# Kernel optimization log

Hardware: AMD Instinct MI355X
Metric: run time of the kernel (lower is better)

Reference implementation:

```python
import jax, jax.numpy as jnp
import numpy as np

IN_F = 128
OUT_F = 64
ALPHA = 0.2  # LeakyReLU negative slope


def setup_inputs() -> dict:
    key = jax.random.key(0)
    k1, k2, k3 = jax.random.split(key, 3)
    B, N = 8, 2048
    inp = jax.random.normal(k1, (B, N, IN_F), dtype=jnp.float32)
    adj = jnp.ones((B, N, N), dtype=jnp.float32)  # unused by the layer (no masking)
    # Parameters (xavier_uniform-style scale)
    w_lim = np.sqrt(6.0 / (IN_F + OUT_F))
    W = jax.random.uniform(k2, (OUT_F, IN_F), minval=-w_lim, maxval=w_lim, dtype=jnp.float32)
    a_lim = np.sqrt(6.0 / (2 * OUT_F + 1))
    a = jax.random.uniform(k3, (1, 2 * OUT_F), minval=-a_lim, maxval=a_lim, dtype=jnp.float32)
    return {"input": inp, "adj": adj, "W": W, "a": a}


def reference(input, adj, W, a):
    # h = W(input): [B, N, OUT_F]
    h = jnp.einsum("bnf,of->bno", input, W)
    # a^T [h_i || h_j] = a1^T h_i + a2^T h_j  (exact decomposition of the concat trick)
    a1 = a[0, :OUT_F]
    a2 = a[0, OUT_F:]
    s1 = jnp.einsum("bno,o->bn", h, a1)  # score contribution from node i
    s2 = jnp.einsum("bno,o->bn", h, a2)  # score contribution from node j
    e = s1[:, :, None] + s2[:, None, :]  # [B, N, N]
    e = jnp.where(e >= 0, e, ALPHA * e)  # LeakyReLU
    attention = jax.nn.softmax(e, axis=2)  # softmax over neighbors j (adj is NOT used)
    h_prime = jnp.einsum("bij,bjo->bio", attention, h)
    # concat=True -> ELU
    return jax.nn.elu(h_prime)
```

## Files before the change

kernel.cpp:

```cpp
#include <hip/hip_runtime.h>
#include <cstdio>

#define ALPHA 0.2f
constexpr int NN = 2048;
constexpr int NB = 8;
constexpr int FI = 128;
constexpr int FO = 64;
constexpr int SEG = 16;
constexpr int NSEG = NN / SEG;

__global__ __launch_bounds__(256) void k_h(const float* __restrict__ inp,
    const float* __restrict__ W, const float* __restrict__ a,
    float* __restrict__ h, float* __restrict__ s1, float* __restrict__ s2)
{
  __shared__ float4 Wq[(FI / 4) * FO];
  const int t = threadIdx.x;
  const float4* Wg = (const float4*)W;
#pragma unroll
  for (int i = 0; i < 8; ++i) {
    int f = t + i * 256;
    Wq[(f & 31) * FO + (f >> 5)] = Wg[f];
  }
  __syncthreads();
  const int lane = t & 63;
  const int wv = t >> 6;
  const size_t rowbase = ((size_t)blockIdx.x * 4 + wv) * 8;
  const float a1v = a[lane], a2v = a[FO + lane];
#pragma unroll
  for (int g = 0; g < 2; ++g) {
    const size_t r0 = rowbase + g * 4;
    const float4* x0 = (const float4*)(inp + r0 * FI);
    const float4* x1 = x0 + (FI / 4);
    const float4* x2 = x0 + 2 * (FI / 4);
    const float4* x3 = x0 + 3 * (FI / 4);
    float acc0 = 0.f, acc1 = 0.f, acc2 = 0.f, acc3 = 0.f;
#pragma unroll
    for (int cq = 0; cq < 32; ++cq) {
      float4 w = Wq[cq * FO + lane];
      float4 xa = x0[cq];
      acc0 = fmaf(xa.x, w.x, fmaf(xa.y, w.y, fmaf(xa.z, w.z, fmaf(xa.w, w.w, acc0))));
      float4 xb = x1[cq];
      acc1 = fmaf(xb.x, w.x, fmaf(xb.y, w.y, fmaf(xb.z, w.z, fmaf(xb.w, w.w, acc1))));
      float4 xc = x2[cq];
      acc2 = fmaf(xc.x, w.x, fmaf(xc.y, w.y, fmaf(xc.z, w.z, fmaf(xc.w, w.w, acc2))));
      float4 xd = x3[cq];
      acc3 = fmaf(xd.x, w.x, fmaf(xd.y, w.y, fmaf(xd.z, w.z, fmaf(xd.w, w.w, acc3))));
    }
    h[(r0 + 0) * FO + lane] = acc0;
    h[(r0 + 1) * FO + lane] = acc1;
    h[(r0 + 2) * FO + lane] = acc2;
    h[(r0 + 3) * FO + lane] = acc3;
    float p0 = acc0 * a1v, q0 = acc0 * a2v;
    float p1 = acc1 * a1v, q1 = acc1 * a2v;
    float p2 = acc2 * a1v, q2 = acc2 * a2v;
    float p3 = acc3 * a1v, q3 = acc3 * a2v;
#pragma unroll
    for (int off = 32; off; off >>= 1) {
      p0 += __shfl_down(p0, off); q0 += __shfl_down(q0, off);
      p1 += __shfl_down(p1, off); q1 += __shfl_down(q1, off);
      p2 += __shfl_down(p2, off); q2 += __shfl_down(q2, off);
      p3 += __shfl_down(p3, off); q3 += __shfl_down(q3, off);
    }
    if (lane == 0) {
      s1[r0 + 0] = p0; s2[r0 + 0] = q0;
      s1[r0 + 1] = p1; s2[r0 + 1] = q1;
      s1[r0 + 2] = p2; s2[r0 + 2] = q2;
      s1[r0 + 3] = p3; s2[r0 + 3] = q3;
    }
  }
}

__global__ __launch_bounds__(512) void k_count(
    const float* __restrict__ s1g, const float* __restrict__ s2g,
    int* __restrict__ sortedIdx, float* __restrict__ epS,
    float* __restrict__ eqS, int* __restrict__ kArr,
    float* __restrict__ zpArr, float* __restrict__ zqArr,
    float* __restrict__ m2g)
{
  __shared__ float sv[NN];
  __shared__ float sepA[NN], seqA[NN];
  __shared__ float wmx[8];
  __shared__ int   prk[64 * 8], pkk[64 * 8];
  __shared__ float pzp[64 * 8], pzq[64 * 8];
  const int b = blockIdx.x >> 5;
  const int c = blockIdx.x & 31;
  const int t = threadIdx.x;
  const int lane = t & 63;
  const int wv = t >> 6;
  float4* sv4 = (float4*)sv;
  const float4* g4 = (const float4*)(s2g + (size_t)b * NN);
  const float4 mine = g4[t];
  sv4[t] = mine;
  float mx = fmaxf(fmaxf(mine.x, mine.y), fmaxf(mine.z, mine.w));
#pragma unroll
  for (int off = 32; off; off >>= 1) mx = fmaxf(mx, __shfl_down(mx, off));
  if (lane == 0) wmx[wv] = mx;
  __syncthreads();
  float m2 = wmx[0];
#pragma unroll
  for (int i = 1; i < 8; ++i) m2 = fmaxf(m2, wmx[i]);
  if (c == 0 && t == 0) m2g[b] = m2;
  {
    float4 e1, e2;
    e1.x = expf(mine.x - m2); e2.x = expf(ALPHA * (mine.x - m2));
    e1.y = expf(mine.y - m2); e2.y = expf(ALPHA * (mine.y - m2));
    e1.z = expf(mine.z - m2); e2.z = expf(ALPHA * (mine.z - m2));
    e1.w = expf(mine.w - m2); e2.w = expf(ALPHA * (mine.w - m2));
    ((float4*)sepA)[t] = e1;
    ((float4*)seqA)[t] = e2;
  }
  __syncthreads();
  const int ib = c * 64 + lane;
  const float v = sv[ib];
  const float thr = -s1g[(size_t)b * NN + ib];
  int cR0 = 0, cR1 = 0, cK0 = 0, cK1 = 0;
  float zp0 = 0.f, zp1 = 0.f, zq0 = 0.f, zq1 = 0.f;
  const float4* svv = (const float4*)sv;
  const float4* epv = (const float4*)sepA;
  const float4* eqv = (const float4*)seqA;
#pragma unroll 4
  for (int j4 = wv * 64; j4 < wv * 64 + 64; ++j4) {
    const float4 x = svv[j4];
    const float4 e1 = epv[j4];
    const float4 e2 = eqv[j4];
    const int j = 4 * j4;
    bool p0 = (x.x >= thr), p1 = (x.y >= thr), p2 = (x.z >= thr), p3 = (x.w >= thr);
    cK0 += p0 + p1; cK1 += p2 + p3;
    zp0 += (p0 ? e1.x : 0.f) + (p1 ? e1.y : 0.f);
    zp1 += (p2 ? e1.z : 0.f) + (p3 ? e1.w : 0.f);
    zq0 += (p0 ? 0.f : e2.x) + (p1 ? 0.f : e2.y);
    zq1 += (p2 ? 0.f : e2.z) + (p3 ? 0.f : e2.w);
    cR0 += ((x.x > v) || (x.x == v && (j + 0) < ib))
         + ((x.y > v) || (x.y == v && (j + 1) < ib));
    cR1 += ((x.z > v) || (x.z == v && (j + 2) < ib))
         + ((x.w > v) || (x.w == v && (j + 3) < ib));
  }
  prk[lane * 8 + wv] = cR0 + cR1;
  pkk[lane * 8 + wv] = cK0 + cK1;
  pzp[lane * 8 + wv] = zp0 + zp1;
  pzq[lane * 8 + wv] = zq0 + zq1;
  __syncthreads();
  if (t < 64) {
    int rank = 0, kk = 0;
    float zps = 0.f, zqs = 0.f;
#pragma unroll
    for (int i2 = 0; i2 < 8; ++i2) {
      rank += prk[t * 8 + i2]; kk += pkk[t * 8 + i2];
      zps += pzp[t * 8 + i2]; zqs += pzq[t * 8 + i2];
    }
    const int i = c * 64 + t;
    kArr[b * NN + i] = kk;
    zpArr[b * NN + i] = zps;
    zqArr[b * NN + i] = zqs;
    sortedIdx[b * NN + rank] = i;
    epS[b * NN + rank] = sepA[i];
    eqS[b * NN + rank] = seqA[i];
  }
}

__global__ __launch_bounds__(256) void k_seg(const float* __restrict__ h,
    const int* __restrict__ sortedIdx, const float* __restrict__ epS,
    const float* __restrict__ eqS,
    float* __restrict__ Lp, float* __restrict__ Lq,
    float* __restrict__ segTotP, float* __restrict__ segTotQ)
{
  const int lane = threadIdx.x & 63;
  const int s = blockIdx.x * 4 + (threadIdx.x >> 6);
  const int b = s >> 7;
  const int base = b * NN + (s & (NSEG - 1)) * SEG;
  float hv[SEG], wp[SEG], wq[SEG];
#pragma unroll
  for (int r = 0; r < SEG; ++r) {
    int idx = sortedIdx[base + r];
    hv[r] = h[((size_t)(b * NN + idx)) * FO + lane];
  }
#pragma unroll
  for (int r = 0; r < SEG; ++r) { wp[r] = epS[base + r]; wq[r] = eqS[base + r]; }
  float run = 0.f;
#pragma unroll
  for (int r = 0; r < SEG; ++r) {
    run = fmaf(wp[r], hv[r], run);
    Lp[(size_t)(base + r) * FO + lane] = run;
  }
  segTotP[(size_t)s * FO + lane] = run;
  run = 0.f;
#pragma unroll
  for (int r = SEG - 1; r >= 0; --r) {
    run = fmaf(wq[r], hv[r], run);
    Lq[(size_t)(base + r) * FO + lane] = run;
  }
  segTotQ[(size_t)s * FO + lane] = run;
}

__global__ __launch_bounds__(256) void k_out(const float* __restrict__ s1g,
    const int* __restrict__ kArr, const float* __restrict__ zpArr,
    const float* __restrict__ zqArr,
    const float* __restrict__ Lp, const float* __restrict__ Lq,
    const float* __restrict__ segTotP, const float* __restrict__ segTotQ,
    const float* __restrict__ m2g, float* __restrict__ out)
{
  __shared__ float cs[NSEG * FO];
  __shared__ float qt[4][FO];
  const int t = threadIdx.x;
  const int b = blockIdx.x >> 5;
  const int c = blockIdx.x & 31;
  const int lane = t & 63;
  const int wv = t >> 6;
  int kk[16];
#pragma unroll
  for (int rr = 0; rr < 16; ++rr)
    kk[rr] = kArr[b * NN + c * 64 + wv * 16 + rr];

  {
    const float4* sv4 = (const float4*)(segTotP + (size_t)b * NSEG * FO);
    float4* csv = (float4*)cs;
#pragma unroll
    for (int i = 0; i < NSEG * FO / 4 / 256; ++i) csv[t + i * 256] = sv4[t + i * 256];
  }
  __syncthreads();
  {
    float run = 0.f;
    for (int s = wv * 32; s < wv * 32 + 32; ++s) { run += cs[s * FO + lane]; cs[s * FO + lane] = run; }
    qt[wv][lane] = run;
  }
  __syncthreads();
  {
    float off = 0.f;
    for (int q2 = 0; q2 < wv; ++q2) off += qt[q2][lane];
    for (int s = wv * 32; s < wv * 32 + 32; ++s) cs[s * FO + lane] += off;
  }
  __syncthreads();
  float P[16];
#pragma unroll
  for (int rr = 0; rr < 16; ++rr) {
    const int k = kk[rr];
    P[rr] = 0.f;
    if (k > 0) {
      const int sP = (k - 1) >> 4;
      P[rr] = (sP > 0 ? cs[(sP - 1) * FO + lane] : 0.f) +
              Lp[((size_t)(b * NN + k - 1)) * FO + lane];
    }
  }
  __syncthreads();

  {
    const float4* sv4 = (const float4*)(segTotQ + (size_t)b * NSEG * FO);
    float4* csv = (float4*)cs;
#pragma unroll
    for (int i = 0; i < NSEG * FO / 4 / 256; ++i) csv[t + i * 256] = sv4[t + i * 256];
  }
  __syncthreads();
  {
    float run = 0.f;
    for (int s = wv * 32 + 31; s >= wv * 32; --s) { run += cs[s * FO + lane]; cs[s * FO + lane] = run; }
    qt[wv][lane] = run;
  }
  __syncthreads();
  {
    float off = 0.f;
    for (int q2 = wv + 1; q2 < 4; ++q2) off += qt[q2][lane];
    for (int s = wv * 32; s < wv * 32 + 32; ++s) cs[s * FO + lane] += off;
  }
  __syncthreads();
  float Q[16];
#pragma unroll
  for (int rr = 0; rr < 16; ++rr) {
    const int k = kk[rr];
    Q[rr] = 0.f;
    if (k < NN) {
      const int sQ = k >> 4;
      Q[rr] = (sQ < NSEG - 1 ? cs[(sQ + 1) * FO + lane] : 0.f) +
              Lq[((size_t)(b * NN + k)) * FO + lane];
    }
  }

  const float m2 = m2g[b];
#pragma unroll
  for (int rr = 0; rr < 16; ++rr) {
    const int i = c * 64 + wv * 16 + rr;
    const int gi = b * NN + i;
    const float u = s1g[gi] + m2;
    const float cmx = fmaxf(u, ALPHA * u);
    const float wp = expf(u - cmx);
    const float wq = expf(ALPHA * u - cmx);
    const float v = (wp * P[rr] + wq * Q[rr]) / (wp * zpArr[gi] + wq * zqArr[gi]);
    out[(size_t)gi * FO + lane] = (v > 0.f) ? v : expm1f(v);
  }
}

extern "C" void kernel_launch(void* const* d_in, const int* in_sizes, int n_in,
                              void* d_out, int out_size, void* d_ws, size_t ws_size,
                              hipStream_t stream) {
  const float* inp = (const float*)d_in[0];
  const float* W = (const float*)d_in[2];
  const float* a = (const float*)d_in[3];
  float* out = (float*)d_out;

  constexpr size_t NH = (size_t)NB * NN * FO;
  constexpr size_t NR = (size_t)NB * NN;
  constexpr size_t NST = (size_t)NB * NSEG * FO;
  constexpr size_t needFloats = 3 * NH + 8 * NR + 2 * NST + 8;
  if (ws_size < needFloats * sizeof(float)) {
    fprintf(stderr, "kernel_launch: ws too small (%zu < %zu)\n",
            ws_size, needFloats * sizeof(float));
    return;
  }
  float* ws = (float*)d_ws;
  float* h        = ws;
  float* Lp       = h + NH;
  float* Lq       = Lp + NH;
  float* s1       = Lq + NH;
  float* s2       = s1 + NR;
  int*   sortedIdx= (int*)(s2 + NR);
  float* epS      = (float*)(sortedIdx + NR);
  float* eqS      = epS + NR;
  int*   kArr     = (int*)(eqS + NR);
  float* zpArr    = (float*)(kArr + NR);
  float* zqArr    = zpArr + NR;
  float* segTotP  = zqArr + NR;
  float* segTotQ  = segTotP + NST;
  float* m2       = segTotQ + NST;

  k_h<<<512, 256, 0, stream>>>(inp, W, a, h, s1, s2);
  k_count<<<256, 512, 0, stream>>>(s1, s2, sortedIdx, epS, eqS,
                                   kArr, zpArr, zqArr, m2);
  k_seg<<<256, 256, 0, stream>>>(h, sortedIdx, epS, eqS, Lp, Lq,
                                 segTotP, segTotQ);
  k_out<<<256, 256, 0, stream>>>(s1, kArr, zpArr, zqArr, Lp, Lq,
                                 segTotP, segTotQ, m2, out);
}
```

Measured before the change: 69.57 us.

## Fold W into attention vectors and compute h inside segment scan kernel

The first kernel now precomputes W^T a1 and W^T a2 so the scores s1/s2 come from a 128-wide dot product per row, without building h. The full projection h is recomputed inside k_seg by gathering input rows in sorted order, which removes the h write and re-read. The per-row softmax normalisers zp/zq, previously accumulated in the O(N^2) count loop, are now taken from prefix and suffix sums of the sorted exp weights. This shrinks the count kernel's inner loop and removes its exp work. The cost is heavier gathered loads of 128-float input rows in k_seg and extra prefix-offset logic in k_out.

```diff
diff --git a/kernel.cpp b/kernel.cpp
--- a/kernel.cpp
+++ b/kernel.cpp
@@ -9,79 +9,50 @@
 constexpr int SEG = 16;
 constexpr int NSEG = NN / SEG;
 
-__global__ __launch_bounds__(256) void k_h(const float* __restrict__ inp,
+__global__ __launch_bounds__(256) void k_s12(const float* __restrict__ inp,
     const float* __restrict__ W, const float* __restrict__ a,
-    float* __restrict__ h, float* __restrict__ s1, float* __restrict__ s2)
+    float* __restrict__ s1, float* __restrict__ s2)
 {
-  __shared__ float4 Wq[(FI / 4) * FO];
+  __shared__ float sw1[FI], sw2[FI];
   const int t = threadIdx.x;
-  const float4* Wg = (const float4*)W;
-#pragma unroll
-  for (int i = 0; i < 8; ++i) {
-    int f = t + i * 256;
-    Wq[(f & 31) * FO + (f >> 5)] = Wg[f];
+  if (t < FI) {
+    float w1 = 0.f, w2 = 0.f;
+    for (int o = 0; o < FO; ++o) {
+      const float wof = W[o * FI + t];
+      w1 = fmaf(a[o], wof, w1);
+      w2 = fmaf(a[FO + o], wof, w2);
+    }
+    sw1[t] = w1; sw2[t] = w2;
   }
   __syncthreads();
   const int lane = t & 63;
   const int wv = t >> 6;
-  const size_t rowbase = ((size_t)blockIdx.x * 4 + wv) * 8;
-  const float a1v = a[lane], a2v = a[FO + lane];
-#pragma unroll
-  for (int g = 0; g < 2; ++g) {
-    const size_t r0 = rowbase + g * 4;
-    const float4* x0 = (const float4*)(inp + r0 * FI);
-    const float4* x1 = x0 + (FI / 4);
-    const float4* x2 = x0 + 2 * (FI / 4);
-    const float4* x3 = x0 + 3 * (FI / 4);
-    float acc0 = 0.f, acc1 = 0.f, acc2 = 0.f, acc3 = 0.f;
-#pragma unroll
-    for (int cq = 0; cq < 32; ++cq) {
-      float4 w = Wq[cq * FO + lane];
-      float4 xa = x0[cq];
-      acc0 = fmaf(xa.x, w.x, fmaf(xa.y, w.y, fmaf(xa.z, w.z, fmaf(xa.w, w.w, acc0))));
-      float4 xb = x1[cq];
-      acc1 = fmaf(xb.x, w.x, fmaf(xb.y, w.y, fmaf(xb.z, w.z, fmaf(xb.w, w.w, acc1))));
-      float4 xc = x2[cq];
-      acc2 = fmaf(xc.x, w.x, fmaf(xc.y, w.y, fmaf(xc.z, w.z, fmaf(xc.w, w.w, acc2))));
-      float4 xd = x3[cq];
-      acc3 = fmaf(xd.x, w.x, fmaf(xd.y, w.y, fmaf(xd.z, w.z, fmaf(xd.w, w.w, acc3))));
-    }
-    h[(r0 + 0) * FO + lane] = acc0;
-    h[(r0 + 1) * FO + lane] = acc1;
-    h[(r0 + 2) * FO + lane] = acc2;
-    h[(r0 + 3) * FO + lane] = acc3;
-    float p0 = acc0 * a1v, q0 = acc0 * a2v;
-    float p1 = acc1 * a1v, q1 = acc1 * a2v;
-    float p2 = acc2 * a1v, q2 = acc2 * a2v;
-    float p3 = acc3 * a1v, q3 = acc3 * a2v;
+  const float w1a = sw1[lane], w1b = sw1[lane + 64];
+  const float w2a = sw2[lane], w2b = sw2[lane + 64];
+  const size_t row0 = (size_t)blockIdx.x * 32 + wv * 8;
+#pragma unroll
+  for (int r = 0; r < 8; ++r) {
+    const float xa = inp[(row0 + r) * FI + lane];
+    const float xb = inp[(row0 + r) * FI + 64 + lane];
+    float p = fmaf(xa, w1a, xb * w1b);
+    float q = fmaf(xa, w2a, xb * w2b);
 #pragma unroll
     for (int off = 32; off; off >>= 1) {
-      p0 += __shfl_down(p0, off); q0 += __shfl_down(q0, off);
-      p1 += __shfl_down(p1, off); q1 += __shfl_down(q1, off);
-      p2 += __shfl_down(p2, off); q2 += __shfl_down(q2, off);
-      p3 += __shfl_down(p3, off); q3 += __shfl_down(q3, off);
-    }
-    if (lane == 0) {
-      s1[r0 + 0] = p0; s2[r0 + 0] = q0;
-      s1[r0 + 1] = p1; s2[r0 + 1] = q1;
-      s1[r0 + 2] = p2; s2[r0 + 2] = q2;
-      s1[r0 + 3] = p3; s2[r0 + 3] = q3;
-    }
+      p += __shfl_down(p, off);
+      q += __shfl_down(q, off);
+    }
+    if (lane == 0) { s1[row0 + r] = p; s2[row0 + r] = q; }
   }
 }
 
 __global__ __launch_bounds__(512) void k_count(
     const float* __restrict__ s1g, const float* __restrict__ s2g,
     int* __restrict__ sortedIdx, float* __restrict__ epS,
-    float* __restrict__ eqS, int* __restrict__ kArr,
-    float* __restrict__ zpArr, float* __restrict__ zqArr,
-    float* __restrict__ m2g)
+    float* __restrict__ eqS, int* __restrict__ kArr, float* __restrict__ m2g)
 {
   __shared__ float sv[NN];
-  __shared__ float sepA[NN], seqA[NN];
   __shared__ float wmx[8];
-  __shared__ int   prk[64 * 8], pkk[64 * 8];
-  __shared__ float pzp[64 * 8], pzq[64 * 8];
+  __shared__ int prk[64 * 8], pkk[64 * 8];
   const int b = blockIdx.x >> 5;
   const int c = blockIdx.x & 31;
   const int t = threadIdx.x;
@@ -100,107 +71,115 @@
 #pragma unroll
   for (int i = 1; i < 8; ++i) m2 = fmaxf(m2, wmx[i]);
   if (c == 0 && t == 0) m2g[b] = m2;
-  {
-    float4 e1, e2;
-    e1.x = expf(mine.x - m2); e2.x = expf(ALPHA * (mine.x - m2));
-    e1.y = expf(mine.y - m2); e2.y = expf(ALPHA * (mine.y - m2));
-    e1.z = expf(mine.z - m2); e2.z = expf(ALPHA * (mine.z - m2));
-    e1.w = expf(mine.w - m2); e2.w = expf(ALPHA * (mine.w - m2));
-    ((float4*)sepA)[t] = e1;
-    ((float4*)seqA)[t] = e2;
-  }
-  __syncthreads();
   const int ib = c * 64 + lane;
   const float v = sv[ib];
   const float thr = -s1g[(size_t)b * NN + ib];
-  int cR0 = 0, cR1 = 0, cK0 = 0, cK1 = 0;
-  float zp0 = 0.f, zp1 = 0.f, zq0 = 0.f, zq1 = 0.f;
+  int cR = 0, cK = 0;
   const float4* svv = (const float4*)sv;
-  const float4* epv = (const float4*)sepA;
-  const float4* eqv = (const float4*)seqA;
 #pragma unroll 4
   for (int j4 = wv * 64; j4 < wv * 64 + 64; ++j4) {
     const float4 x = svv[j4];
-    const float4 e1 = epv[j4];
-    const float4 e2 = eqv[j4];
     const int j = 4 * j4;
-    bool p0 = (x.x >= thr), p1 = (x.y >= thr), p2 = (x.z >= thr), p3 = (x.w >= thr);
-    cK0 += p0 + p1; cK1 += p2 + p3;
-    zp0 += (p0 ? e1.x : 0.f) + (p1 ? e1.y : 0.f);
-    zp1 += (p2 ? e1.z : 0.f) + (p3 ? e1.w : 0.f);
-    zq0 += (p0 ? 0.f : e2.x) + (p1 ? 0.f : e2.y);
-    zq1 += (p2 ? 0.f : e2.z) + (p3 ? 0.f : e2.w);
-    cR0 += ((x.x > v) || (x.x == v && (j + 0) < ib))
-         + ((x.y > v) || (x.y == v && (j + 1) < ib));
-    cR1 += ((x.z > v) || (x.z == v && (j + 2) < ib))
-         + ((x.w > v) || (x.w == v && (j + 3) < ib));
-  }
-  prk[lane * 8 + wv] = cR0 + cR1;
-  pkk[lane * 8 + wv] = cK0 + cK1;
-  pzp[lane * 8 + wv] = zp0 + zp1;
-  pzq[lane * 8 + wv] = zq0 + zq1;
+    cK += (x.x >= thr) + (x.y >= thr) + (x.z >= thr) + (x.w >= thr);
+    cR += ((x.x > v) || (x.x == v && (j + 0) < ib))
+        + ((x.y > v) || (x.y == v && (j + 1) < ib))
+        + ((x.z > v) || (x.z == v && (j + 2) < ib))
+        + ((x.w > v) || (x.w == v && (j + 3) < ib));
+  }
+  prk[lane * 8 + wv] = cR;
+  pkk[lane * 8 + wv] = cK;
   __syncthreads();
   if (t < 64) {
     int rank = 0, kk = 0;
-    float zps = 0.f, zqs = 0.f;
-#pragma unroll
-    for (int i2 = 0; i2 < 8; ++i2) {
-      rank += prk[t * 8 + i2]; kk += pkk[t * 8 + i2];
-      zps += pzp[t * 8 + i2]; zqs += pzq[t * 8 + i2];
-    }
+#pragma unroll
+    for (int i2 = 0; i2 < 8; ++i2) { rank += prk[t * 8 + i2]; kk += pkk[t * 8 + i2]; }
     const int i = c * 64 + t;
+    const float vv = sv[i];
     kArr[b * NN + i] = kk;
-    zpArr[b * NN + i] = zps;
-    zqArr[b * NN + i] = zqs;
     sortedIdx[b * NN + rank] = i;
-    epS[b * NN + rank] = sepA[i];
-    eqS[b * NN + rank] = seqA[i];
-  }
-}
-
-__global__ __launch_bounds__(256) void k_seg(const float* __restrict__ h,
-    const int* __restrict__ sortedIdx, const float* __restrict__ epS,
-    const float* __restrict__ eqS,
+    epS[b * NN + rank] = expf(vv - m2);
+    eqS[b * NN + rank] = expf(ALPHA * (vv - m2));
+  }
+}
+
+__global__ __launch_bounds__(256) void k_seg(const float* __restrict__ inp,
+    const float* __restrict__ W, const int* __restrict__ sortedIdx,
+    const float* __restrict__ epS, const float* __restrict__ eqS,
     float* __restrict__ Lp, float* __restrict__ Lq,
-    float* __restrict__ segTotP, float* __restrict__ segTotQ)
+    float* __restrict__ segTotP, float* __restrict__ segTotQ,
+    float* __restrict__ epPre, float* __restrict__ eqSuf,
+    float* __restrict__ segEp, float* __restrict__ segEq)
 {
-  const int lane = threadIdx.x & 63;
-  const int s = blockIdx.x * 4 + (threadIdx.x >> 6);
+  __shared__ float4 Wq[(FI / 4) * FO];
+  const int t = threadIdx.x;
+  const float4* Wg = (const float4*)W;
+#pragma unroll
+  for (int i = 0; i < 8; ++i) {
+    int f = t + i * 256;
+    Wq[(f & 31) * FO + (f >> 5)] = Wg[f];
+  }
+  __syncthreads();
+  const int lane = t & 63;
+  const int s = blockIdx.x * 4 + (t >> 6);
   const int b = s >> 7;
   const int base = b * NN + (s & (NSEG - 1)) * SEG;
-  float hv[SEG], wp[SEG], wq[SEG];
-#pragma unroll
-  for (int r = 0; r < SEG; ++r) {
-    int idx = sortedIdx[base + r];
-    hv[r] = h[((size_t)(b * NN + idx)) * FO + lane];
-  }
+  const float* xb = inp + (size_t)b * NN * FI;
+  const float* xp[SEG];
+#pragma unroll
+  for (int r = 0; r < SEG; ++r) xp[r] = xb + (size_t)sortedIdx[base + r] * FI;
+  float acc[SEG];
+#pragma unroll
+  for (int r = 0; r < SEG; ++r) acc[r] = 0.f;
+#pragma unroll 4
+  for (int cq = 0; cq < FI / 4; ++cq) {
+    const float4 w = Wq[cq * FO + lane];
+#pragma unroll
+    for (int r = 0; r < SEG; ++r) {
+      const float4 xv = *(const float4*)(xp[r] + 4 * cq);
+      acc[r] = fmaf(xv.x, w.x, fmaf(xv.y, w.y, fmaf(xv.z, w.z, fmaf(xv.w, w.w, acc[r]))));
+    }
+  }
+  float wp[SEG], wq[SEG];
 #pragma unroll
   for (int r = 0; r < SEG; ++r) { wp[r] = epS[base + r]; wq[r] = eqS[base + r]; }
   float run = 0.f;
 #pragma unroll
   for (int r = 0; r < SEG; ++r) {
-    run = fmaf(wp[r], hv[r], run);
+    run = fmaf(wp[r], acc[r], run);
     Lp[(size_t)(base + r) * FO + lane] = run;
   }
   segTotP[(size_t)s * FO + lane] = run;
   run = 0.f;
 #pragma unroll
   for (int r = SEG - 1; r >= 0; --r) {
-    run = fmaf(wq[r], hv[r], run);
+    run = fmaf(wq[r], acc[r], run);
     Lq[(size_t)(base + r) * FO + lane] = run;
   }
   segTotQ[(size_t)s * FO + lane] = run;
+  float pp = 0.f, qq = 0.f;
+#pragma unroll
+  for (int r = 0; r < SEG; ++r) pp += (r <= lane) ? wp[r] : 0.f;
+#pragma unroll
+  for (int r = 0; r < SEG; ++r) qq += (r >= lane) ? wq[r] : 0.f;
+  if (lane < SEG) {
+    epPre[base + lane] = pp;
+    eqSuf[base + lane] = qq;
+  }
+  if (lane == SEG - 1) segEp[s] = pp;
+  if (lane == 0) segEq[s] = qq;
 }
 
 __global__ __launch_bounds__(256) void k_out(const float* __restrict__ s1g,
-    const int* __restrict__ kArr, const float* __restrict__ zpArr,
-    const float* __restrict__ zqArr,
+    const int* __restrict__ kArr,
     const float* __restrict__ Lp, const float* __restrict__ Lq,
     const float* __restrict__ segTotP, const float* __restrict__ segTotQ,
+    const float* __restrict__ epPre, const float* __restrict__ eqSuf,
+    const float* __restrict__ segEp, const float* __restrict__ segEq,
     const float* __restrict__ m2g, float* __restrict__ out)
 {
   __shared__ float cs[NSEG * FO];
   __shared__ float qt[4][FO];
+  __shared__ float sEp[NSEG], sEq[NSEG], sOffP[NSEG], sOffQ[NSEG];
   const int t = threadIdx.x;
   const int b = blockIdx.x >> 5;
   const int c = blockIdx.x & 31;
@@ -210,6 +189,10 @@
 #pragma unroll
   for (int rr = 0; rr < 16; ++rr)
     kk[rr] = kArr[b * NN + c * 64 + wv * 16 + rr];
+  if (t < NSEG) {
+    sEp[t] = segEp[b * NSEG + t];
+    sEq[t] = segEq[b * NSEG + t];
+  }
 
   {
     const float4* sv4 = (const float4*)(segTotP + (size_t)b * NSEG * FO);
@@ -218,6 +201,14 @@
     for (int i = 0; i < NSEG * FO / 4 / 256; ++i) csv[t + i * 256] = sv4[t + i * 256];
   }
   __syncthreads();
+  if (t < NSEG) {
+    float accp = 0.f;
+    for (int s2 = 0; s2 < t; ++s2) accp += sEp[s2];
+    sOffP[t] = accp;
+    float accq = 0.f;
+    for (int s2 = t + 1; s2 < NSEG; ++s2) accq += sEq[s2];
+    sOffQ[t] = accq;
+  }
   {
     float run = 0.f;
     for (int s = wv * 32; s < wv * 32 + 32; ++s) { run += cs[s * FO + lane]; cs[s * FO + lane] = run; }
@@ -279,11 +270,14 @@
   for (int rr = 0; rr < 16; ++rr) {
     const int i = c * 64 + wv * 16 + rr;
     const int gi = b * NN + i;
+    const int k = kk[rr];
     const float u = s1g[gi] + m2;
     const float cmx = fmaxf(u, ALPHA * u);
     const float wp = expf(u - cmx);
     const float wq = expf(ALPHA * u - cmx);
-    const float v = (wp * P[rr] + wq * Q[rr]) / (wp * zpArr[gi] + wq * zqArr[gi]);
+    const float zp = (k > 0)  ? sOffP[(k - 1) >> 4] + epPre[(size_t)b * NN + k - 1] : 0.f;
+    const float zq = (k < NN) ? sOffQ[k >> 4] + eqSuf[(size_t)b * NN + k] : 0.f;
+    const float v = (wp * P[rr] + wq * Q[rr]) / (wp * zp + wq * zq);
     out[(size_t)gi * FO + lane] = (v > 0.f) ? v : expm1f(v);
   }
 }
@@ -299,15 +293,15 @@
   constexpr size_t NH = (size_t)NB * NN * FO;
   constexpr size_t NR = (size_t)NB * NN;
   constexpr size_t NST = (size_t)NB * NSEG * FO;
-  constexpr size_t needFloats = 3 * NH + 8 * NR + 2 * NST + 8;
+  constexpr size_t NSC = (size_t)NB * NSEG;
+  constexpr size_t needFloats = 2 * NH + 8 * NR + 2 * NST + 2 * NSC + 8;
   if (ws_size < needFloats * sizeof(float)) {
     fprintf(stderr, "kernel_launch: ws too small (%zu < %zu)\n",
             ws_size, needFloats * sizeof(float));
     return;
   }
   float* ws = (float*)d_ws;
-  float* h        = ws;
-  float* Lp       = h + NH;
+  float* Lp       = ws;
   float* Lq       = Lp + NH;
   float* s1       = Lq + NH;
   float* s2       = s1 + NR;
@@ -315,17 +309,18 @@
   float* epS      = (float*)(sortedIdx + NR);
   float* eqS      = epS + NR;
   int*   kArr     = (int*)(eqS + NR);
-  float* zpArr    = (float*)(kArr + NR);
-  float* zqArr    = zpArr + NR;
-  float* segTotP  = zqArr + NR;
+  float* epPre    = (float*)(kArr + NR);
+  float* eqSuf    = epPre + NR;
+  float* segTotP  = eqSuf + NR;
   float* segTotQ  = segTotP + NST;
-  float* m2       = segTotQ + NST;
-
-  k_h<<<512, 256, 0, stream>>>(inp, W, a, h, s1, s2);
-  k_count<<<256, 512, 0, stream>>>(s1, s2, sortedIdx, epS, eqS,
-                                   kArr, zpArr, zqArr, m2);
-  k_seg<<<256, 256, 0, stream>>>(h, sortedIdx, epS, eqS, Lp, Lq,
-                                 segTotP, segTotQ);
-  k_out<<<256, 256, 0, stream>>>(s1, kArr, zpArr, zqArr, Lp, Lq,
-                                 segTotP, segTotQ, m2, out);
-}
+  float* segEp    = segTotQ + NST;
+  float* segEq    = segEp + NSC;
+  float* m2       = segEq + NSC;
+
+  k_s12<<<512, 256, 0, stream>>>(inp, W, a, s1, s2);
+  k_count<<<256, 512, 0, stream>>>(s1, s2, sortedIdx, epS, eqS, kArr, m2);
+  k_seg<<<256, 256, 0, stream>>>(inp, W, sortedIdx, epS, eqS, Lp, Lq,
+                                 segTotP, segTotQ, epPre, eqSuf, segEp, segEq);
+  k_out<<<256, 256, 0, stream>>>(s1, kArr, Lp, Lq, segTotP, segTotQ,
+                                 epPre, eqSuf, segEp, segEq, m2, out);
+}
```

Result: slower. 86.61 us (+24.5%).
